# Kernel tuning notes

Measured on AMD Instinct MI355X. Metric: run time of the kernel, lower is better.

## Reference

```python
import jax, jax.numpy as jnp
import numpy as np

B, C, H, W = 64, 64, 64, 64  # C = num_features (time + C-1 space dims)
EPS = 1e-5  # module eps; also used as numerical clamp like the torch manifold


def setup_inputs() -> dict:
    key = jax.random.key(0)
    k1, k2 = jax.random.split(key)
    # Valid Lorentz (k=1) points: x0 = sqrt(1 + ||x_space||^2)
    xs = 0.5 * jax.random.normal(k1, (B, C - 1, H, W), dtype=jnp.float32)
    x0 = jnp.sqrt(1.0 + jnp.sum(xs * xs, axis=1, keepdims=True))
    x = jnp.concatenate([x0, xs], axis=1)  # [B, C, H, W]
    gamma = 0.5 + jax.random.uniform(k2, (C - 1,), dtype=jnp.float32)
    beta = 0.05 * jax.random.normal(jax.random.fold_in(key, 7), (C - 1,), dtype=jnp.float32)
    return {"x": x, "gamma": gamma, "beta": beta}


def reference(x, gamma, beta):
    Bn, Cn, Hn, Wn = x.shape
    xf = x.transpose(0, 2, 3, 1).reshape(-1, Cn)  # [N, C], N = B*H*W

    # Lorentz midpoint (centroid): mean, then normalize by Lorentz norm
    m = jnp.mean(xf, axis=0)                      # [C]
    mm = m[0] * m[0] - jnp.sum(m[1:] * m[1:])     # -<m,m>_L (positive for timelike)
    mu = m / jnp.sqrt(jnp.maximum(mm, EPS))       # [C], on hyperboloid

    # alpha = -<x, mu>_L  (>= 1 on the manifold)
    alpha = xf[:, 0] * mu[0] - xf[:, 1:] @ mu[1:]          # [N]
    alpha = jnp.maximum(alpha, 1.0 + EPS)

    # geodesic distance & Frechet variance
    d = jnp.arccosh(alpha)                                  # [N]
    var = jnp.mean(d * d)

    # logmap at mu: v = d/sqrt(alpha^2-1) * (x - alpha*mu)
    coef = d / jnp.sqrt(alpha * alpha - 1.0)
    v = coef[:, None] * (xf - alpha[:, None] * mu[None, :])  # [N, C]

    # parallel transport mu -> origin o=(1,0,...):
    # PT(v) = v + <o,v>_L/(1 - <mu,o>_L) * (mu + o) = v - v0/(1+mu0) * (mu + o)
    mu_plus_o = mu.at[0].add(1.0)
    vo = v - (v[:, 0] / (1.0 + mu[0]))[:, None] * mu_plus_o[None, :]

    # scale/shift space components, then orthogonal projection back to manifold
    vs = vo[:, 1:]                                           # [N, C-1]
    s = gamma[None, :] * vs / (jnp.sqrt(var) + EPS) + beta[None, :]
    t = jnp.sqrt(1.0 + jnp.sum(s * s, axis=1, keepdims=True))
    out = jnp.concatenate([t, s], axis=1)                    # [N, C]

    return out.reshape(Bn, Hn, Wn, Cn).transpose(0, 3, 1, 2)
```

## Files before the change

kernel.cpp:

```cpp
#include <hip/hip_runtime.h>
#include <math.h>

#define BDIM 64
#define CDIM 64
#define HWN  4096
#define NROWS (BDIM * HWN)
#define EPSV 1e-5f

#define WS_SUMS 0
#define WS_MU   64
#define WS_VAR  128

__global__ __launch_bounds__(256) void k_chansum(const float* __restrict__ x,
                                                 float* __restrict__ ws) {
    const int plane = blockIdx.x;
    const int c = plane & (CDIM - 1);
    const float4* p4 = reinterpret_cast<const float4*>(x + (size_t)plane * HWN);
    float s = 0.f;
#pragma unroll
    for (int i = 0; i < HWN / 4 / 256; ++i) {
        float4 v = p4[threadIdx.x + i * 256];
        s += (v.x + v.y) + (v.z + v.w);
    }
    for (int off = 32; off; off >>= 1) s += __shfl_down(s, off, 64);
    __shared__ float red[4];
    const int lane = threadIdx.x & 63, wid = threadIdx.x >> 6;
    if (lane == 0) red[wid] = s;
    __syncthreads();
    if (threadIdx.x == 0)
        atomicAdd(&ws[WS_SUMS + c], (red[0] + red[1]) + (red[2] + red[3]));
}

__global__ void k_mu(float* __restrict__ ws) {
    const int c = threadIdx.x;
    const float m = ws[WS_SUMS + c] * (1.0f / (float)NROWS);
    float mm = (c == 0) ? m * m : -m * m;
    for (int off = 32; off; off >>= 1) mm += __shfl_down(mm, off, 64);
    mm = __shfl(mm, 0, 64);
    ws[WS_MU + c] = m / sqrtf(fmaxf(mm, EPSV));
}

__global__ __launch_bounds__(256) void k_var(const float* __restrict__ x,
                                             float* __restrict__ ws) {
    __shared__ float smu[CDIM];
    if (threadIdx.x < CDIM) smu[threadIdx.x] = ws[WS_MU + threadIdx.x];
    __syncthreads();

    const int n = blockIdx.x * 256 + threadIdx.x;
    const int b = n >> 12;
    const int hw = n & (HWN - 1);
    const float* p = x + (size_t)b * CDIM * HWN + hw;

    float alpha = p[0] * smu[0];
#pragma unroll
    for (int c = 1; c < CDIM; ++c) alpha -= p[(size_t)c * HWN] * smu[c];
    alpha = fmaxf(alpha, 1.0f + EPSV);
    const float d = acoshf(alpha);
    float dd = d * d;

    for (int off = 32; off; off >>= 1) dd += __shfl_down(dd, off, 64);
    __shared__ float red[4];
    const int lane = threadIdx.x & 63, wid = threadIdx.x >> 6;
    if (lane == 0) red[wid] = dd;
    __syncthreads();
    if (threadIdx.x == 0)
        atomicAdd(&ws[WS_VAR], (red[0] + red[1]) + (red[2] + red[3]));
}

__global__ __launch_bounds__(256) void k_out(const float* __restrict__ x,
                                             const float* __restrict__ gamma,
                                             const float* __restrict__ beta,
                                             float* __restrict__ out,
                                             const float* __restrict__ ws) {
    __shared__ float smu[CDIM], sg[CDIM], sb[CDIM];
    if (threadIdx.x < CDIM) {
        smu[threadIdx.x] = ws[WS_MU + threadIdx.x];
        sg[threadIdx.x] = (threadIdx.x >= 1) ? gamma[threadIdx.x - 1] : 0.f;
        sb[threadIdx.x] = (threadIdx.x >= 1) ? beta[threadIdx.x - 1] : 0.f;
    }
    __syncthreads();

    const float var = ws[WS_VAR] * (1.0f / (float)NROWS);
    const float inv_sv = 1.0f / (sqrtf(var) + EPSV);

    const int n = blockIdx.x * 256 + threadIdx.x;
    const int b = n >> 12;
    const int hw = n & (HWN - 1);
    const size_t base = (size_t)b * CDIM * HWN + hw;
    const float* p = x + base;

    float xr[CDIM];
#pragma unroll
    for (int c = 0; c < CDIM; ++c) xr[c] = p[(size_t)c * HWN];

    float alpha = xr[0] * smu[0];
#pragma unroll
    for (int c = 1; c < CDIM; ++c) alpha -= xr[c] * smu[c];
    alpha = fmaxf(alpha, 1.0f + EPSV);
    const float d = acoshf(alpha);
    const float coef = d / sqrtf(alpha * alpha - 1.0f);

    const float v0 = coef * (xr[0] - alpha * smu[0]);
    const float k = v0 / (1.0f + smu[0]);

    float* op = out + base;
    float s2 = 0.f;
#pragma unroll
    for (int c = 1; c < CDIM; ++c) {
        const float v = coef * (xr[c] - alpha * smu[c]);
        const float vo = v - k * smu[c];
        const float s = sg[c] * vo * inv_sv + sb[c];
        s2 += s * s;
        op[(size_t)c * HWN] = s;
    }
    op[0] = sqrtf(1.0f + s2);
}

extern "C" void kernel_launch(void* const* d_in, const int* in_sizes, int n_in,
                              void* d_out, int out_size, void* d_ws, size_t ws_size,
                              hipStream_t stream) {
    const float* x     = (const float*)d_in[0];
    const float* gamma = (const float*)d_in[1];
    const float* beta  = (const float*)d_in[2];
    float* out = (float*)d_out;
    float* ws  = (float*)d_ws;

    hipMemsetAsync(ws, 0, 1024, stream);

    k_chansum<<<BDIM * CDIM, 256, 0, stream>>>(x, ws);
    k_mu<<<1, 64, 0, stream>>>(ws);
    k_var<<<NROWS / 256, 256, 0, stream>>>(x, ws);
    k_out<<<NROWS / 256, 256, 0, stream>>>(x, gamma, beta, out, ws);
}
```

Before: 165.3 us.

## Drop atomics and mu kernel, cache alpha/coef, vectorize pixel processing by four

Per-plane channel sums and per-block variance partials are now written to distinct workspace slots instead of atomics. This removes the memset and the single-thread-block mu kernel, and each block recomputes mu redundantly. Alpha and the logmap coefficient are stored in the first pass and reloaded in the output pass, so the output kernel no longer recomputes the 64-channel dot product and acosh. Each thread now handles four adjacent pixels with float4 loads and stores, at the cost of extra workspace traffic and fewer blocks.

```diff
diff --git a/kernel.cpp b/kernel.cpp
--- a/kernel.cpp
+++ b/kernel.cpp
@@ -5,16 +5,16 @@
 #define CDIM 64
 #define HWN  4096
 #define NROWS (BDIM * HWN)
+#define CHSTRIDE (CDIM * HWN)
 #define EPSV 1e-5f
 
-#define WS_SUMS 0
-#define WS_MU   64
-#define WS_VAR  128
+#define DD_OFF    4096
+#define ALPHA_OFF 8192
+#define COEF_OFF  (ALPHA_OFF + NROWS)
 
 __global__ __launch_bounds__(256) void k_chansum(const float* __restrict__ x,
                                                  float* __restrict__ ws) {
     const int plane = blockIdx.x;
-    const int c = plane & (CDIM - 1);
     const float4* p4 = reinterpret_cast<const float4*>(x + (size_t)plane * HWN);
     float s = 0.f;
 #pragma unroll
@@ -27,36 +27,62 @@
     const int lane = threadIdx.x & 63, wid = threadIdx.x >> 6;
     if (lane == 0) red[wid] = s;
     __syncthreads();
-    if (threadIdx.x == 0)
-        atomicAdd(&ws[WS_SUMS + c], (red[0] + red[1]) + (red[2] + red[3]));
+    if (threadIdx.x == 0) ws[plane] = (red[0] + red[1]) + (red[2] + red[3]);
 }
 
-__global__ void k_mu(float* __restrict__ ws) {
-    const int c = threadIdx.x;
-    const float m = ws[WS_SUMS + c] * (1.0f / (float)NROWS);
-    float mm = (c == 0) ? m * m : -m * m;
-    for (int off = 32; off; off >>= 1) mm += __shfl_down(mm, off, 64);
-    mm = __shfl(mm, 0, 64);
-    ws[WS_MU + c] = m / sqrtf(fmaxf(mm, EPSV));
+__device__ __forceinline__ void compute_mu(const float* __restrict__ ws,
+                                           float* smu, float* stmp) {
+    const int t = threadIdx.x, c = t & 63, g = t >> 6;
+    float m = 0.f;
+#pragma unroll
+    for (int b = 0; b < BDIM / 4; ++b) m += ws[(g * (BDIM / 4) + b) * CDIM + c];
+    stmp[g * 64 + c] = m;
+    __syncthreads();
+    if (t < 64) {
+        const float msum = (stmp[c] + stmp[64 + c]) + (stmp[128 + c] + stmp[192 + c]);
+        const float mval = msum * (1.0f / (float)NROWS);
+        float mm = (c == 0) ? mval * mval : -mval * mval;
+        for (int off = 32; off; off >>= 1) mm += __shfl_down(mm, off, 64);
+        mm = __shfl(mm, 0, 64);
+        smu[c] = mval / sqrtf(fmaxf(mm, EPSV));
+    }
+    __syncthreads();
 }
 
-__global__ __launch_bounds__(256) void k_var(const float* __restrict__ x,
-                                             float* __restrict__ ws) {
-    __shared__ float smu[CDIM];
-    if (threadIdx.x < CDIM) smu[threadIdx.x] = ws[WS_MU + threadIdx.x];
-    __syncthreads();
+__global__ __launch_bounds__(256) void k_alpha(const float* __restrict__ x,
+                                               float* __restrict__ ws) {
+    __shared__ float smu[64];
+    __shared__ float stmp[256];
+    compute_mu(ws, smu, stmp);
 
-    const int n = blockIdx.x * 256 + threadIdx.x;
-    const int b = n >> 12;
-    const int hw = n & (HWN - 1);
-    const float* p = x + (size_t)b * CDIM * HWN + hw;
+    const int tid = blockIdx.x * 256 + threadIdx.x;
+    const int n0 = tid * 4;
+    const int b = n0 >> 12;
+    const int hw = n0 & (HWN - 1);
+    const float* p = x + (size_t)b * CHSTRIDE + hw;
 
-    float alpha = p[0] * smu[0];
+    float al[4];
+    {
+        const float4 v = *reinterpret_cast<const float4*>(p);
+        const float m0 = smu[0];
+        al[0] = v.x * m0; al[1] = v.y * m0; al[2] = v.z * m0; al[3] = v.w * m0;
+    }
 #pragma unroll
-    for (int c = 1; c < CDIM; ++c) alpha -= p[(size_t)c * HWN] * smu[c];
-    alpha = fmaxf(alpha, 1.0f + EPSV);
-    const float d = acoshf(alpha);
-    float dd = d * d;
+    for (int c = 1; c < CDIM; ++c) {
+        const float4 v = *reinterpret_cast<const float4*>(p + (size_t)c * HWN);
+        const float m = smu[c];
+        al[0] -= v.x * m; al[1] -= v.y * m; al[2] -= v.z * m; al[3] -= v.w * m;
+    }
+    float dd = 0.f, co[4];
+#pragma unroll
+    for (int j = 0; j < 4; ++j) {
+        al[j] = fmaxf(al[j], 1.0f + EPSV);
+        const float d = acoshf(al[j]);
+        dd += d * d;
+        co[j] = d / sqrtf(al[j] * al[j] - 1.0f);
+    }
+    *reinterpret_cast<float4*>(&ws[ALPHA_OFF + n0]) = make_float4(al[0], al[1], al[2], al[3]);
+    *reinterpret_cast<float4*>(&ws[COEF_OFF + n0])  = make_float4(co[0], co[1], co[2], co[3]);
 
     for (int off = 32; off; off >>= 1) dd += __shfl_down(dd, off, 64);
     __shared__ float red[4];
@@ -64,7 +90,7 @@
     if (lane == 0) red[wid] = dd;
     __syncthreads();
     if (threadIdx.x == 0)
-        atomicAdd(&ws[WS_VAR], (red[0] + red[1]) + (red[2] + red[3]));
+        ws[DD_OFF + blockIdx.x] = (red[0] + red[1]) + (red[2] + red[3]);
 }
 
 __global__ __launch_bounds__(256) void k_out(const float* __restrict__ x,
@@ -72,48 +98,70 @@
                                              const float* __restrict__ beta,
                                              float* __restrict__ out,
                                              const float* __restrict__ ws) {
-    __shared__ float smu[CDIM], sg[CDIM], sb[CDIM];
-    if (threadIdx.x < CDIM) {
-        smu[threadIdx.x] = ws[WS_MU + threadIdx.x];
+    __shared__ float smu[64], sg[64], sb[64];
+    __shared__ float stmp[256];
+    compute_mu(ws, smu, stmp);
+
+    float pd = ws[DD_OFF + threadIdx.x];
+    for (int off = 32; off; off >>= 1) pd += __shfl_down(pd, off, 64);
+    const int lane = threadIdx.x & 63, wid = threadIdx.x >> 6;
+    if (lane == 0) stmp[wid] = pd;
+    if (threadIdx.x < 64) {
         sg[threadIdx.x] = (threadIdx.x >= 1) ? gamma[threadIdx.x - 1] : 0.f;
         sb[threadIdx.x] = (threadIdx.x >= 1) ? beta[threadIdx.x - 1] : 0.f;
     }
     __syncthreads();
-
-    const float var = ws[WS_VAR] * (1.0f / (float)NROWS);
+    const float varsum = (stmp[0] + stmp[1]) + (stmp[2] + stmp[3]);
+    const float var = varsum * (1.0f / (float)NROWS);
     const float inv_sv = 1.0f / (sqrtf(var) + EPSV);
 
-    const int n = blockIdx.x * 256 + threadIdx.x;
-    const int b = n >> 12;
-    const int hw = n & (HWN - 1);
-    const size_t base = (size_t)b * CDIM * HWN + hw;
+    const int tid = blockIdx.x * 256 + threadIdx.x;
+    const int n0 = tid * 4;
+    const int b = n0 >> 12;
+    const int hw = n0 & (HWN - 1);
+    const size_t base = (size_t)b * CHSTRIDE + hw;
     const float* p = x + base;
+    float* op = out + base;
 
-    float xr[CDIM];
+    float al[4], co[4];
+    {
+        const float4 a4 = *reinterpret_cast<const float4*>(&ws[ALPHA_OFF + n0]);
+        const float4 c4 = *reinterpret_cast<const float4*>(&ws[COEF_OFF + n0]);
+        al[0] = a4.x; al[1] = a4.y; al[2] = a4.z; al[3] = a4.w;
+        co[0] = c4.x; co[1] = c4.y; co[2] = c4.z; co[3] = c4.w;
+    }
+
+    float kk[4];
+    {
+        const float4 v = *reinterpret_cast<const float4*>(p);
+        const float xv[4] = {v.x, v.y, v.z, v.w};
+        const float m0 = smu[0];
+        const float inv1m0 = 1.0f / (1.0f + m0);
 #pragma unroll
-    for (int c = 0; c < CDIM; ++c) xr[c] = p[(size_t)c * HWN];
+        for (int j = 0; j < 4; ++j)
+            kk[j] = co[j] * (xv[j] - al[j] * m0) * inv1m0;
+    }
 
-    float alpha = xr[0] * smu[0];
-#pragma unroll
-    for (int c = 1; c < CDIM; ++c) alpha -= xr[c] * smu[c];
-    alpha = fmaxf(alpha, 1.0f + EPSV);
-    const float d = acoshf(alpha);
-    const float coef = d / sqrtf(alpha * alpha - 1.0f);
-
-    const float v0 = coef * (xr[0] - alpha * smu[0]);
-    const float k = v0 / (1.0f + smu[0]);
-
-    float* op = out + base;
-    float s2 = 0.f;
+    float s2[4] = {0.f, 0.f, 0.f, 0.f};
 #pragma unroll
     for (int c = 1; c < CDIM; ++c) {
-        const float v = coef * (xr[c] - alpha * smu[c]);
-        const float vo = v - k * smu[c];
-        const float s = sg[c] * vo * inv_sv + sb[c];
-        s2 += s * s;
-        op[(size_t)c * HWN] = s;
+        const float4 v = *reinterpret_cast<const float4*>(p + (size_t)c * HWN);
+        const float xv[4] = {v.x, v.y, v.z, v.w};
+        const float m = smu[c], g = sg[c], bb = sb[c];
+        float sv[4];
+#pragma unroll
+        for (int j = 0; j < 4; ++j) {
+            const float vv = co[j] * (xv[j] - al[j] * m);
+            const float vo = vv - kk[j] * m;
+            sv[j] = g * vo * inv_sv + bb;
+            s2[j] += sv[j] * sv[j];
+        }
+        *reinterpret_cast<float4*>(op + (size_t)c * HWN) =
+            make_float4(sv[0], sv[1], sv[2], sv[3]);
     }
-    op[0] = sqrtf(1.0f + s2);
+    *reinterpret_cast<float4*>(op) =
+        make_float4(sqrtf(1.0f + s2[0]), sqrtf(1.0f + s2[1]),
+                    sqrtf(1.0f + s2[2]), sqrtf(1.0f + s2[3]));
 }
 
 extern "C" void kernel_launch(void* const* d_in, const int* in_sizes, int n_in,
@@ -125,10 +173,7 @@
     float* out = (float*)d_out;
     float* ws  = (float*)d_ws;
 
-    hipMemsetAsync(ws, 0, 1024, stream);
-
     k_chansum<<<BDIM * CDIM, 256, 0, stream>>>(x, ws);
-    k_mu<<<1, 64, 0, stream>>>(ws);
-    k_var<<<NROWS / 256, 256, 0, stream>>>(x, ws);
-    k_out<<<NROWS / 256, 256, 0, stream>>>(x, gamma, beta, out, ws);
+    k_alpha<<<NROWS / 4 / 256, 256, 0, stream>>>(x, ws);
+    k_out<<<NROWS / 4 / 256, 256, 0, stream>>>(x, gamma, beta, out, ws);
 }
```

Result: faster. 138.3 us (-16.3%).

## Drop memset and mu kernel, use deterministic partials, cache alpha/coef

Applied to the files above, without the earlier changes.

Removes the workspace memset and the single-block mu kernel. Channel sums and per-block variance partials are now written to distinct slots instead of atomics, and each consumer block recomputes mu and the variance from those partials. The alpha pass stores per-row alpha and coef to workspace so the output kernel skips the 64-channel dot product and acosh, at the cost of extra 2 MB of writes and reads. Every block redundantly reduces the partial arrays.

```diff
diff --git a/kernel.cpp b/kernel.cpp
--- a/kernel.cpp
+++ b/kernel.cpp
@@ -5,16 +5,18 @@
 #define CDIM 64
 #define HWN  4096
 #define NROWS (BDIM * HWN)
+#define CHSTRIDE (CDIM * HWN)
 #define EPSV 1e-5f
 
-#define WS_SUMS 0
-#define WS_MU   64
-#define WS_VAR  128
+#define ROWBLOCKS (NROWS / 256)
+
+#define DD_OFF    4096
+#define ALPHA_OFF 8192
+#define COEF_OFF  (ALPHA_OFF + NROWS)
 
 __global__ __launch_bounds__(256) void k_chansum(const float* __restrict__ x,
                                                  float* __restrict__ ws) {
     const int plane = blockIdx.x;
-    const int c = plane & (CDIM - 1);
     const float4* p4 = reinterpret_cast<const float4*>(x + (size_t)plane * HWN);
     float s = 0.f;
 #pragma unroll
@@ -27,44 +29,56 @@
     const int lane = threadIdx.x & 63, wid = threadIdx.x >> 6;
     if (lane == 0) red[wid] = s;
     __syncthreads();
-    if (threadIdx.x == 0)
-        atomicAdd(&ws[WS_SUMS + c], (red[0] + red[1]) + (red[2] + red[3]));
+    if (threadIdx.x == 0) ws[plane] = (red[0] + red[1]) + (red[2] + red[3]);
 }
 
-__global__ void k_mu(float* __restrict__ ws) {
-    const int c = threadIdx.x;
-    const float m = ws[WS_SUMS + c] * (1.0f / (float)NROWS);
-    float mm = (c == 0) ? m * m : -m * m;
-    for (int off = 32; off; off >>= 1) mm += __shfl_down(mm, off, 64);
-    mm = __shfl(mm, 0, 64);
-    ws[WS_MU + c] = m / sqrtf(fmaxf(mm, EPSV));
+__device__ __forceinline__ void compute_mu(const float* __restrict__ ws,
+                                           float* smu, float* stmp) {
+    const int t = threadIdx.x, c = t & 63, g = t >> 6;
+    float m = 0.f;
+#pragma unroll
+    for (int b = 0; b < BDIM / 4; ++b) m += ws[(g * (BDIM / 4) + b) * CDIM + c];
+    stmp[g * 64 + c] = m;
+    __syncthreads();
+    if (t < 64) {
+        const float msum = (stmp[c] + stmp[64 + c]) + (stmp[128 + c] + stmp[192 + c]);
+        const float mval = msum * (1.0f / (float)NROWS);
+        float mm = (c == 0) ? mval * mval : -mval * mval;
+        for (int off = 32; off; off >>= 1) mm += __shfl_down(mm, off, 64);
+        mm = __shfl(mm, 0, 64);
+        smu[c] = mval / sqrtf(fmaxf(mm, EPSV));
+    }
+    __syncthreads();
 }
 
-__global__ __launch_bounds__(256) void k_var(const float* __restrict__ x,
-                                             float* __restrict__ ws) {
-    __shared__ float smu[CDIM];
-    if (threadIdx.x < CDIM) smu[threadIdx.x] = ws[WS_MU + threadIdx.x];
-    __syncthreads();
+__global__ __launch_bounds__(256) void k_alpha(const float* __restrict__ x,
+                                               float* __restrict__ ws) {
+    __shared__ float smu[64];
+    __shared__ float stmp[256];
+    compute_mu(ws, smu, stmp);
 
     const int n = blockIdx.x * 256 + threadIdx.x;
     const int b = n >> 12;
     const int hw = n & (HWN - 1);
-    const float* p = x + (size_t)b * CDIM * HWN + hw;
+    const float* p = x + (size_t)b * CHSTRIDE + hw;
 
     float alpha = p[0] * smu[0];
 #pragma unroll
     for (int c = 1; c < CDIM; ++c) alpha -= p[(size_t)c * HWN] * smu[c];
     alpha = fmaxf(alpha, 1.0f + EPSV);
     const float d = acoshf(alpha);
+    const float coef = d / sqrtf(alpha * alpha - 1.0f);
+    ws[ALPHA_OFF + n] = alpha;
+    ws[COEF_OFF + n]  = coef;
+
     float dd = d * d;
-
     for (int off = 32; off; off >>= 1) dd += __shfl_down(dd, off, 64);
     __shared__ float red[4];
     const int lane = threadIdx.x & 63, wid = threadIdx.x >> 6;
     if (lane == 0) red[wid] = dd;
     __syncthreads();
     if (threadIdx.x == 0)
-        atomicAdd(&ws[WS_VAR], (red[0] + red[1]) + (red[2] + red[3]));
+        ws[DD_OFF + blockIdx.x] = (red[0] + red[1]) + (red[2] + red[3]);
 }
 
 __global__ __launch_bounds__(256) void k_out(const float* __restrict__ x,
@@ -72,43 +86,43 @@
                                              const float* __restrict__ beta,
                                              float* __restrict__ out,
                                              const float* __restrict__ ws) {
-    __shared__ float smu[CDIM], sg[CDIM], sb[CDIM];
-    if (threadIdx.x < CDIM) {
-        smu[threadIdx.x] = ws[WS_MU + threadIdx.x];
+    __shared__ float smu[64], sg[64], sb[64];
+    __shared__ float stmp[256];
+    compute_mu(ws, smu, stmp);
+
+    float pd = ws[DD_OFF + threadIdx.x] + ws[DD_OFF + 256 + threadIdx.x] +
+               ws[DD_OFF + 512 + threadIdx.x] + ws[DD_OFF + 768 + threadIdx.x];
+    for (int off = 32; off; off >>= 1) pd += __shfl_down(pd, off, 64);
+    const int lane = threadIdx.x & 63, wid = threadIdx.x >> 6;
+    if (lane == 0) stmp[wid] = pd;
+    if (threadIdx.x < 64) {
         sg[threadIdx.x] = (threadIdx.x >= 1) ? gamma[threadIdx.x - 1] : 0.f;
         sb[threadIdx.x] = (threadIdx.x >= 1) ? beta[threadIdx.x - 1] : 0.f;
     }
     __syncthreads();
-
-    const float var = ws[WS_VAR] * (1.0f / (float)NROWS);
+    const float varsum = (stmp[0] + stmp[1]) + (stmp[2] + stmp[3]);
+    const float var = varsum * (1.0f / (float)NROWS);
     const float inv_sv = 1.0f / (sqrtf(var) + EPSV);
 
     const int n = blockIdx.x * 256 + threadIdx.x;
     const int b = n >> 12;
     const int hw = n & (HWN - 1);
-    const size_t base = (size_t)b * CDIM * HWN + hw;
+    const size_t base = (size_t)b * CHSTRIDE + hw;
     const float* p = x + base;
+    float* op = out + base;
 
-    float xr[CDIM];
-#pragma unroll
-    for (int c = 0; c < CDIM; ++c) xr[c] = p[(size_t)c * HWN];
+    const float al = ws[ALPHA_OFF + n];
+    const float co = ws[COEF_OFF + n];
+    const float m0 = smu[0];
+    const float kk = co * (p[0] - al * m0) / (1.0f + m0);
 
-    float alpha = xr[0] * smu[0];
-#pragma unroll
-    for (int c = 1; c < CDIM; ++c) alpha -= xr[c] * smu[c];
-    alpha = fmaxf(alpha, 1.0f + EPSV);
-    const float d = acoshf(alpha);
-    const float coef = d / sqrtf(alpha * alpha - 1.0f);
-
-    const float v0 = coef * (xr[0] - alpha * smu[0]);
-    const float k = v0 / (1.0f + smu[0]);
-
-    float* op = out + base;
     float s2 = 0.f;
 #pragma unroll
     for (int c = 1; c < CDIM; ++c) {
-        const float v = coef * (xr[c] - alpha * smu[c]);
-        const float vo = v - k * smu[c];
+        const float xv = p[(size_t)c * HWN];
+        const float m = smu[c];
+        const float v = co * (xv - al * m);
+        const float vo = v - kk * m;
         const float s = sg[c] * vo * inv_sv + sb[c];
         s2 += s * s;
         op[(size_t)c * HWN] = s;
@@ -125,10 +139,7 @@
     float* out = (float*)d_out;
     float* ws  = (float*)d_ws;
 
-    hipMemsetAsync(ws, 0, 1024, stream);
-
     k_chansum<<<BDIM * CDIM, 256, 0, stream>>>(x, ws);
-    k_mu<<<1, 64, 0, stream>>>(ws);
-    k_var<<<NROWS / 256, 256, 0, stream>>>(x, ws);
-    k_out<<<NROWS / 256, 256, 0, stream>>>(x, gamma, beta, out, ws);
+    k_alpha<<<ROWBLOCKS, 256, 0, stream>>>(x, ws);
+    k_out<<<ROWBLOCKS, 256, 0, stream>>>(x, gamma, beta, out, ws);
 }
```

After: 137.8 us. 16.7% less time.
